# Performance work log

Hardware: AMD Instinct MI355X
Metric: run time of the kernel (lower is better)

## Reference

```python
import jax, jax.numpy as jnp
import numpy as np

B, IN_UNITS, IN_CHANNELS, NUM_UNITS, UNIT_SIZE = 256, 8, 1152, 10, 16
NUM_ITERS = 3


def setup_inputs() -> dict:
    key = jax.random.key(0)
    k1, k2 = jax.random.split(key)
    x = jax.random.normal(k1, (B, IN_UNITS, IN_CHANNELS), dtype=jnp.float32)
    # W from nn.Parameter(torch.randn(1, in_channels, num_units, unit_size, in_units)); drop leading 1
    W = jax.random.normal(k2, (IN_CHANNELS, NUM_UNITS, UNIT_SIZE, IN_UNITS), dtype=jnp.float32)
    return {"x": x, "W": W}


def reference(x, W):
    # x: [B, in_units=i, in_channels=j]; original transposes to [B, j, i]
    # u_hat = W @ x : [B, j, n, u]
    batch = x.shape[0]
    u_hat = jnp.einsum('jnui,bij->bjnu', W, x)
    b = jnp.zeros((IN_CHANNELS, NUM_UNITS), dtype=x.dtype)  # b_ij [j, n]
    v = None
    for _ in range(NUM_ITERS):
        # legacy F.softmax on 4D [1,j,n,1] -> dim=1 = in_channels axis
        c = jax.nn.softmax(b, axis=0)  # [j, n]
        s = jnp.einsum('jn,bjnu->bnu', c, u_hat)  # s_j: [B, n, u]
        # squash over dim=2 of [B,1,n,u,1] == num_units axis (axis=1 here)
        mag_sq = jnp.sum(s * s, axis=1, keepdims=True)  # [B, 1, u]
        v = (mag_sq / (1.0 + mag_sq)) * (s / jnp.sqrt(mag_sq))  # [B, n, u]
        # agreement: mean over batch of <u_hat, v>
        b = b + jnp.einsum('bjnu,bnu->jn', u_hat, v) / batch
    return v[..., None]  # [B, num_units, unit_size, 1] == v_j.squeeze(1)
```

## Files before the change

kernel.cpp:

```cpp
#include <hip/hip_runtime.h>
#include <stdint.h>

#define B   256
#define IU  8
#define JC  1152
#define NN  10
#define UU  16
#define NU  160
#define JN  11520
#define WROW 1280
#define NP  9216
#define KB  36

typedef short bf16x8 __attribute__((ext_vector_type(8)));
typedef float f32x4  __attribute__((ext_vector_type(4)));

__device__ __forceinline__ short f2bf(float f) {
    union { float f; uint32_t u; } cv; cv.f = f;
    uint32_t u = cv.u;
    uint32_t r = u + 0x7fffu + ((u >> 16) & 1u);
    return (short)(r >> 16);
}
__device__ __forceinline__ float bf2f(short h) {
    union { uint32_t u; float f; } cv; cv.u = ((uint32_t)(unsigned short)h) << 16;
    return cv.f;
}
__device__ __forceinline__ uint32_t bfbits(float f) {
    union { float f; uint32_t u; } cv; cv.f = f;
    return (cv.u + 0x7fffu + ((cv.u >> 16) & 1u)) >> 16;
}
__device__ __forceinline__ uint32_t pk2(float a, float b) {
    return bfbits(a) | (bfbits(b) << 16);
}
__device__ __forceinline__ void gload16(const void* g, void* l) {
    __builtin_amdgcn_global_load_lds(
        (const __attribute__((address_space(1))) void*)g,
        (__attribute__((address_space(3))) void*)l, 16, 0, 0);
}

__global__ void __launch_bounds__(256)
k_prep(const float* __restrict__ xg, const float* __restrict__ wg,
       short* __restrict__ wbf, short* __restrict__ xbf) {
    const int bid = blockIdx.x, tid = threadIdx.x;
    if (bid < 576) {
        const int jt = bid % 18, rt = bid / 18;
        const int j0 = jt * 64, r0 = rt * 64;
        __shared__ short T[64][72];
        #pragma unroll
        for (int p = 0; p < 4; ++p) {
            int idx = tid + 256 * p;
            int row = idx >> 4;
            int c4  = (idx & 15) * 4;
            float4 xv = *reinterpret_cast<const float4*>(
                &xg[(size_t)(r0 + row) * JC + j0 + c4]);
            T[c4+0][row] = f2bf(xv.x);
            T[c4+1][row] = f2bf(xv.y);
            T[c4+2][row] = f2bf(xv.z);
            T[c4+3][row] = f2bf(xv.w);
        }
        __syncthreads();
        #pragma unroll
        for (int p = 0; p < 2; ++p) {
            int idx = tid + 256 * p;
            int jl = idx >> 3;
            int r8 = (idx & 7) * 8;
            uint4 d = *reinterpret_cast<const uint4*>(&T[jl][r8]);
            *reinterpret_cast<uint4*>(&xbf[(size_t)(j0 + jl) * 2048 + r0 + r8]) = d;
        }
    } else {
        const int b2 = bid - 576;
        size_t base = (size_t)b2 * 2048 + (size_t)tid * 8;
        float4 f0 = *reinterpret_cast<const float4*>(&wg[base]);
        float4 f1 = *reinterpret_cast<const float4*>(&wg[base + 4]);
        uint4 d;
        d.x = pk2(f0.x, f0.y); d.y = pk2(f0.z, f0.w);
        d.z = pk2(f1.x, f1.y); d.w = pk2(f1.z, f1.w);
        *reinterpret_cast<uint4*>(&wbf[base]) = d;
    }
}

__global__ void __launch_bounds__(256, 2)
k_gemm1(const short* __restrict__ xbf, const short* __restrict__ wbf,
        float* __restrict__ s_part) {
    const int kb = blockIdx.x, mt = blockIdx.y;
    const int tid = threadIdx.x;
    const int wv = tid >> 6, lane = tid & 63;
    const int q = lane >> 4, l16 = lane & 15;
    const int b0 = mt * 32;
    const int jb0 = kb * 32;
    const int mfrag = wv >> 1;
    const int ntb = (wv & 1) * 5;

    __shared__ __align__(16) short As[8 * 32 * 8];
    __shared__ __align__(16) short Bs[8 * 160 * 8];

    f32x4 acc[5];
    #pragma unroll
    for (int nt = 0; nt < 5; ++nt) acc[nt] = (f32x4){0.f, 0.f, 0.f, 0.f};

    for (int jc = 0; jc < 4; ++jc) {
        const int j0 = jb0 + jc * 8;
        __syncthreads();
        gload16(xbf + ((size_t)(j0 + (tid >> 5)) * 2048 + (size_t)(b0 + (tid & 31)) * 8),
                &As[tid * 8]);
        const short* wsrc = wbf + (size_t)j0 * WROW;
        #pragma unroll
        for (int p = 0; p < 5; ++p) {
            int ridx = tid + 256 * p;
            gload16(wsrc + (size_t)ridx * 8, &Bs[ridx * 8]);
        }
        __syncthreads();
        #pragma unroll
        for (int s = 0; s < 2; ++s) {
            int jj = s * 4 + q;
            bf16x8 av = *reinterpret_cast<const bf16x8*>(
                &As[(jj * 32 + mfrag * 16 + l16) << 3]);
            #pragma unroll
            for (int nt = 0; nt < 5; ++nt) {
                bf16x8 bv = *reinterpret_cast<const bf16x8*>(
                    &Bs[(jj * 160 + (ntb + nt) * 16 + l16) << 3]);
                acc[nt] = __builtin_amdgcn_mfma_f32_16x16x32_bf16(av, bv, acc[nt], 0, 0, 0);
            }
        }
    }
    float* dst = s_part + (size_t)(kb * 8 + mt) * 5120;
    #pragma unroll
    for (int nt = 0; nt < 5; ++nt)
        #pragma unroll
        for (int reg = 0; reg < 4; ++reg)
            dst[(mfrag * 16 + q * 4 + reg) * 160 + (ntb + nt) * 16 + l16] = acc[nt][reg];
}

__global__ void __launch_bounds__(320, 2)
k_reduce_s(const float* __restrict__ s_part, float* __restrict__ vdst,
           const float* __restrict__ expsum, int t0) {
    const int b = blockIdx.x, tid = threadIdx.x;
    const int t = tid % 160, kq = tid / 160;
    const int mt = b >> 5, bl = b & 31;
    const size_t off = (size_t)mt * 5120 + bl * 160 + t;

    __shared__ float invn[NN];
    if (tid < NN) invn[tid] = t0 ? (1.f / (float)JC) : 1.f / expsum[tid];

    float s = 0.f;
    for (int r = 0; r < 18; ++r)
        s += s_part[(size_t)(kq * 18 + r) * 40960 + off];

    __shared__ float red[2][160];
    __shared__ float sv[NU];
    __shared__ float fb[UU];
    red[kq][t] = s;
    __syncthreads();
    if (tid < NU) sv[tid] = (red[0][tid] + red[1][tid]) * invn[tid >> 4];
    __syncthreads();
    if (tid < UU) {
        float m = 0.f;
        #pragma unroll
        for (int n = 0; n < NN; ++n) { float z = sv[n*16 + tid]; m = fmaf(z, z, m); }
        fb[tid] = sqrtf(m) / (1.f + m);
    }
    __syncthreads();
    if (tid < NU)
        vdst[(size_t)b * NU + tid] = sv[tid] * fb[tid & 15];
}

__global__ void __launch_bounds__(256, 2)
k_vxg(const float* __restrict__ vg, const float* __restrict__ xg,
      float* __restrict__ G, float* __restrict__ expsum) {
    const int np0 = blockIdx.x * 64, m0 = blockIdx.y * 32;
    const int tid = threadIdx.x;
    const int wv = tid >> 6, lane = tid & 63;
    const int q = lane >> 4, l16 = lane & 15;

    if (blockIdx.x == 0 && blockIdx.y == 0 && tid < NN) expsum[tid] = 0.f;

    __shared__ __align__(16) short Ash[8 * 32 * 8];
    __shared__ __align__(16) short Asl[8 * 32 * 8];
    __shared__ __align__(16) short Bsh[8 * 64 * 8];
    __shared__ __align__(16) short Bsl[8 * 64 * 8];

    f32x4 acc[2];
    acc[0] = (f32x4){0.f,0.f,0.f,0.f};
    acc[1] = (f32x4){0.f,0.f,0.f,0.f};

    for (int ks = 0; ks < 4; ++ks) {
        const int b0 = ks * 64;
        __syncthreads();
        #pragma unroll
        for (int p = 0; p < 8; ++p) {
            int idx = tid + 256 * p;
            int bb = idx >> 5, ml = idx & 31;
            float vv = vg[(size_t)(b0 + bb) * NU + m0 + ml];
            short hi = f2bf(vv);
            short lo = f2bf(vv - bf2f(hi));
            int a = ((bb >> 3) * 32 + ml) * 8 + (bb & 7);
            Ash[a] = hi; Asl[a] = lo;
        }
        #pragma unroll
        for (int p = 0; p < 16; ++p) {
            int idx = tid + 256 * p;
            int bb = idx >> 6, nl = idx & 63;
            float xv = xg[(size_t)(b0 + bb) * NP + np0 + nl];
            short hi = f2bf(xv);
            short lo = f2bf(xv - bf2f(hi));
            int a = ((bb >> 3) * 64 + nl) * 8 + (bb & 7);
            Bsh[a] = hi; Bsl[a] = lo;
        }
        __syncthreads();
        #pragma unroll
        for (int s = 0; s < 2; ++s) {
            int kc = s*4 + q;
            bf16x8 bh = *reinterpret_cast<const bf16x8*>(&Bsh[((kc*64 + wv*16 + l16) << 3)]);
            bf16x8 bl = *reinterpret_cast<const bf16x8*>(&Bsl[((kc*64 + wv*16 + l16) << 3)]);
            #pragma unroll
            for (int mtl = 0; mtl < 2; ++mtl) {
                bf16x8 ah = *reinterpret_cast<const bf16x8*>(&Ash[((kc*32 + mtl*16 + l16) << 3)]);
                bf16x8 al = *reinterpret_cast<const bf16x8*>(&Asl[((kc*32 + mtl*16 + l16) << 3)]);
                acc[mtl] = __builtin_amdgcn_mfma_f32_16x16x32_bf16(ah, bh, acc[mtl], 0, 0, 0);
                acc[mtl] = __builtin_amdgcn_mfma_f32_16x16x32_bf16(ah, bl, acc[mtl], 0, 0, 0);
                acc[mtl] = __builtin_amdgcn_mfma_f32_16x16x32_bf16(al, bh, acc[mtl], 0, 0, 0);
            }
        }
    }
    #pragma unroll
    for (int mtl = 0; mtl < 2; ++mtl)
        #pragma unroll
        for (int reg = 0; reg < 4; ++reg) {
            int m  = m0 + mtl*16 + q*4 + reg;
            G[(size_t)m * NP + np0 + wv*16 + l16] = acc[mtl][reg];
        }
}

__global__ void k_wg_db(const float* __restrict__ wg, const float* __restrict__ G,
                        float* __restrict__ blog, short* __restrict__ wbf,
                        float* __restrict__ expsum, int t0) {
    const int j0 = blockIdx.x * 64, n = blockIdx.y;
    const int tid = threadIdx.x;
    const int jl = tid & 63, up = tid >> 6;
    const int j = j0 + jl;

    const float4* wp = reinterpret_cast<const float4*>(
        wg + (size_t)j * WROW + n * 128 + up * 32);
    float4 w[8];
    #pragma unroll
    for (int k = 0; k < 8; ++k) w[k] = wp[k];

    float acc = 0.f;
    #pragma unroll
    for (int q4 = 0; q4 < 4; ++q4) {
        int u = up*4 + q4;
        const float* gp = G + (size_t)(n*16 + u) * NP + j;
        float4 w0 = w[q4*2], w1 = w[q4*2 + 1];
        acc = fmaf(w0.x, gp[0*JC], acc);
        acc = fmaf(w0.y, gp[1*JC], acc);
        acc = fmaf(w0.z, gp[2*JC], acc);
        acc = fmaf(w0.w, gp[3*JC], acc);
        acc = fmaf(w1.x, gp[4*JC], acc);
        acc = fmaf(w1.y, gp[5*JC], acc);
        acc = fmaf(w1.z, gp[6*JC], acc);
        acc = fmaf(w1.w, gp[7*JC], acc);
    }
    __shared__ float red[4][64];
    __shared__ float esh[64];
    __shared__ __align__(16) short Wsh[64][136];
    red[up][jl] = acc;
    __syncthreads();
    if (tid < 64) {
        int jj = j0 + tid;
        float d = (red[0][tid] + red[1][tid] + red[2][tid] + red[3][tid])
                  * (1.f / (float)B);
        float nb = t0 ? d : (blog[jj*NN + n] + d);
        blog[jj*NN + n] = nb;
        float e = __expf(nb);
        esh[tid] = e;
        float s = e;
        s += __shfl_xor(s, 1);  s += __shfl_xor(s, 2);
        s += __shfl_xor(s, 4);  s += __shfl_xor(s, 8);
        s += __shfl_xor(s, 16); s += __shfl_xor(s, 32);
        if (tid == 0) atomicAdd(&expsum[n], s);
    }
    __syncthreads();
    const float e = esh[jl];
    #pragma unroll
    for (int q4 = 0; q4 < 4; ++q4) {
        float4 a = w[q4*2], bq = w[q4*2 + 1];
        uint4 d;
        d.x = pk2(a.x * e, a.y * e);
        d.y = pk2(a.z * e, a.w * e);
        d.z = pk2(bq.x * e, bq.y * e);
        d.w = pk2(bq.z * e, bq.w * e);
        *reinterpret_cast<uint4*>(&Wsh[jl][up*32 + q4*8]) = d;
    }
    __syncthreads();
    #pragma unroll
    for (int p = 0; p < 4; ++p) {
        int idx = tid + 256 * p;
        int jj = idx >> 4, seg = idx & 15;
        uint4 d = *reinterpret_cast<const uint4*>(&Wsh[jj][seg * 8]);
        *reinterpret_cast<uint4*>(&wbf[(size_t)(j0 + jj) * WROW + n*128 + seg*8]) = d;
    }
}

extern "C" void kernel_launch(void* const* d_in, const int* in_sizes, int n_in,
                              void* d_out, int out_size, void* d_ws, size_t ws_size,
                              hipStream_t stream) {
    const float* x = (const float*)d_in[0];
    const float* w = (const float*)d_in[1];
    float* out = (float*)d_out;

    float* ws     = (float*)d_ws;
    float* blog   = ws;
    float* expsum = blog + JN;
    float* v      = expsum + 16;
    short* wbf    = (short*)(v + (size_t)B * NU);
    short* xbf    = wbf + (size_t)JC * WROW;
    float* s_part = (float*)(xbf + (size_t)JC * 2048);
    float* G      = s_part;

    k_prep<<<1296, 256, 0, stream>>>(x, w, wbf, xbf);
    for (int t = 0; t < 3; ++t) {
        k_gemm1<<<dim3(KB, 8), 256, 0, stream>>>(xbf, wbf, s_part);
        k_reduce_s<<<B, 320, 0, stream>>>(s_part, (t == 2) ? out : v, expsum,
                                          (t == 0) ? 1 : 0);
        if (t < 2) {
            k_vxg<<<dim3(144, 5), 256, 0, stream>>>(v, x, G, expsum);
            k_wg_db<<<dim3(18, 10), 256, 0, stream>>>(w, G, blog, wbf, expsum,
                                                      (t == 0) ? 1 : 0);
        }
    }
}
```

Before: 144.1 us.

## Fuse reduction stages into producer kernels via atomic counter grid barriers

```diff
diff --git a/kernel.cpp b/kernel.cpp
--- a/kernel.cpp
+++ b/kernel.cpp
@@ -40,8 +40,9 @@
 
 __global__ void __launch_bounds__(256)
 k_prep(const float* __restrict__ xg, const float* __restrict__ wg,
-       short* __restrict__ wbf, short* __restrict__ xbf) {
+       short* __restrict__ wbf, short* __restrict__ xbf, int* __restrict__ cnt) {
     const int bid = blockIdx.x, tid = threadIdx.x;
+    if (bid == 0 && tid < 32) cnt[tid] = 0;
     if (bid < 576) {
         const int jt = bid % 18, rt = bid / 18;
         const int j0 = jt * 64, r0 = rt * 64;
@@ -80,8 +81,9 @@
 }
 
 __global__ void __launch_bounds__(256, 2)
-k_gemm1(const short* __restrict__ xbf, const short* __restrict__ wbf,
-        float* __restrict__ s_part) {
+k_gemmred(const short* __restrict__ xbf, const short* __restrict__ wbf,
+          float* __restrict__ s_part, float* __restrict__ vdst,
+          const float* __restrict__ expsum, int* __restrict__ cnt, int t0) {
     const int kb = blockIdx.x, mt = blockIdx.y;
     const int tid = threadIdx.x;
     const int wv = tid >> 6, lane = tid & 63;
@@ -91,8 +93,9 @@
     const int mfrag = wv >> 1;
     const int ntb = (wv & 1) * 5;
 
-    __shared__ __align__(16) short As[8 * 32 * 8];
-    __shared__ __align__(16) short Bs[8 * 160 * 8];
+    __shared__ __align__(16) char smem[24576];
+    short* As = (short*)smem;
+    short* Bs = As + 2048;
 
     f32x4 acc[5];
     #pragma unroll
@@ -129,55 +132,58 @@
         #pragma unroll
         for (int reg = 0; reg < 4; ++reg)
             dst[(mfrag * 16 + q * 4 + reg) * 160 + (ntb + nt) * 16 + l16] = acc[nt][reg];
-}
-
-__global__ void __launch_bounds__(320, 2)
-k_reduce_s(const float* __restrict__ s_part, float* __restrict__ vdst,
-           const float* __restrict__ expsum, int t0) {
-    const int b = blockIdx.x, tid = threadIdx.x;
-    const int t = tid % 160, kq = tid / 160;
-    const int mt = b >> 5, bl = b & 31;
-    const size_t off = (size_t)mt * 5120 + bl * 160 + t;
-
-    __shared__ float invn[NN];
-    if (tid < NN) invn[tid] = t0 ? (1.f / (float)JC) : 1.f / expsum[tid];
-
-    float s = 0.f;
-    for (int r = 0; r < 18; ++r)
-        s += s_part[(size_t)(kq * 18 + r) * 40960 + off];
-
-    __shared__ float red[2][160];
-    __shared__ float sv[NU];
-    __shared__ float fb[UU];
-    red[kq][t] = s;
-    __syncthreads();
-    if (tid < NU) sv[tid] = (red[0][tid] + red[1][tid]) * invn[tid >> 4];
+
+    __syncthreads();
+    if (tid == 0)
+        __hip_atomic_fetch_add(&cnt[mt], 1, __ATOMIC_RELEASE, __HIP_MEMORY_SCOPE_AGENT);
+    if (kb >= 32) return;
+    if (tid == 0) {
+        while (__hip_atomic_load(&cnt[mt], __ATOMIC_ACQUIRE, __HIP_MEMORY_SCOPE_AGENT) < KB)
+            __builtin_amdgcn_s_sleep(4);
+    }
+    __syncthreads();
+
+    float* sv  = (float*)smem;
+    float* fbv = sv + 160;
+    if (tid < NU) {
+        float ssum = 0.f;
+        const float* sp = s_part + (size_t)mt * 5120 + (size_t)kb * 160 + tid;
+        #pragma unroll 4
+        for (int r = 0; r < KB; ++r)
+            ssum += sp[(size_t)r * 40960];
+        float inv = t0 ? (1.f / (float)JC) : 1.f / expsum[tid >> 4];
+        sv[tid] = ssum * inv;
+    }
     __syncthreads();
     if (tid < UU) {
         float m = 0.f;
         #pragma unroll
         for (int n = 0; n < NN; ++n) { float z = sv[n*16 + tid]; m = fmaf(z, z, m); }
-        fb[tid] = sqrtf(m) / (1.f + m);
+        fbv[tid] = sqrtf(m) / (1.f + m);
     }
     __syncthreads();
     if (tid < NU)
-        vdst[(size_t)b * NU + tid] = sv[tid] * fb[tid & 15];
-}
-
-__global__ void __launch_bounds__(256, 2)
-k_vxg(const float* __restrict__ vg, const float* __restrict__ xg,
-      float* __restrict__ G, float* __restrict__ expsum) {
+        vdst[(size_t)(mt * 32 + kb) * NU + tid] = sv[tid] * fbv[tid & 15];
+}
+
+__global__ void __launch_bounds__(256, 3)
+k_vxgdb(const float* __restrict__ vg, const float* __restrict__ xg,
+        const float* __restrict__ wg, float* __restrict__ G,
+        float* __restrict__ blog, short* __restrict__ wbf,
+        float* __restrict__ expsum, int* __restrict__ cnt, int t0) {
     const int np0 = blockIdx.x * 64, m0 = blockIdx.y * 32;
+    const int fid = blockIdx.y * 144 + blockIdx.x;
     const int tid = threadIdx.x;
     const int wv = tid >> 6, lane = tid & 63;
     const int q = lane >> 4, l16 = lane & 15;
 
-    if (blockIdx.x == 0 && blockIdx.y == 0 && tid < NN) expsum[tid] = 0.f;
-
-    __shared__ __align__(16) short Ash[8 * 32 * 8];
-    __shared__ __align__(16) short Asl[8 * 32 * 8];
-    __shared__ __align__(16) short Bsh[8 * 64 * 8];
-    __shared__ __align__(16) short Bsl[8 * 64 * 8];
+    __shared__ __align__(16) char smem[24576];
+    short* Ash = (short*)smem;
+    short* Asl = Ash + 2048;
+    short* Bsh = Asl + 2048;
+    short* Bsl = Bsh + 4096;
+
+    if (fid == 0 && tid < NN) expsum[tid] = 0.f;
 
     f32x4 acc[2];
     acc[0] = (f32x4){0.f,0.f,0.f,0.f};
@@ -210,12 +216,12 @@
         #pragma unroll
         for (int s = 0; s < 2; ++s) {
             int kc = s*4 + q;
-            bf16x8 bh = *reinterpret_cast<const bf16x8*>(&Bsh[((kc*64 + wv*16 + l16) << 3)]);
-            bf16x8 bl = *reinterpret_cast<const bf16x8*>(&Bsl[((kc*64 + wv*16 + l16) << 3)]);
+            bf16x8 bh = *reinterpret_cast<const bf16x8*>(&Bsh[(kc*64 + wv*16 + l16) << 3]);
+            bf16x8 bl = *reinterpret_cast<const bf16x8*>(&Bsl[(kc*64 + wv*16 + l16) << 3]);
             #pragma unroll
             for (int mtl = 0; mtl < 2; ++mtl) {
-                bf16x8 ah = *reinterpret_cast<const bf16x8*>(&Ash[((kc*32 + mtl*16 + l16) << 3)]);
-                bf16x8 al = *reinterpret_cast<const bf16x8*>(&Asl[((kc*32 + mtl*16 + l16) << 3)]);
+                bf16x8 ah = *reinterpret_cast<const bf16x8*>(&Ash[(kc*32 + mtl*16 + l16) << 3]);
+                bf16x8 al = *reinterpret_cast<const bf16x8*>(&Asl[(kc*32 + mtl*16 + l16) << 3]);
                 acc[mtl] = __builtin_amdgcn_mfma_f32_16x16x32_bf16(ah, bh, acc[mtl], 0, 0, 0);
                 acc[mtl] = __builtin_amdgcn_mfma_f32_16x16x32_bf16(ah, bl, acc[mtl], 0, 0, 0);
                 acc[mtl] = __builtin_amdgcn_mfma_f32_16x16x32_bf16(al, bh, acc[mtl], 0, 0, 0);
@@ -229,15 +235,24 @@
             int m  = m0 + mtl*16 + q*4 + reg;
             G[(size_t)m * NP + np0 + wv*16 + l16] = acc[mtl][reg];
         }
-}
-
-__global__ void k_wg_db(const float* __restrict__ wg, const float* __restrict__ G,
-                        float* __restrict__ blog, short* __restrict__ wbf,
-                        float* __restrict__ expsum, int t0) {
-    const int j0 = blockIdx.x * 64, n = blockIdx.y;
-    const int tid = threadIdx.x;
+
+    __syncthreads();
+    if (tid == 0)
+        __hip_atomic_fetch_add(cnt, 1, __ATOMIC_RELEASE, __HIP_MEMORY_SCOPE_AGENT);
+    if (fid >= 180) return;
+    if (tid == 0) {
+        while (__hip_atomic_load(cnt, __ATOMIC_ACQUIRE, __HIP_MEMORY_SCOPE_AGENT) < 720)
+            __builtin_amdgcn_s_sleep(4);
+    }
+    __syncthreads();
+
+    const int j0 = (fid % 18) * 64, n = fid / 18;
     const int jl = tid & 63, up = tid >> 6;
     const int j = j0 + jl;
+
+    short* Wsh = (short*)smem;
+    float* red = (float*)(smem + 17408);
+    float* esh = red + 256;
 
     const float4* wp = reinterpret_cast<const float4*>(
         wg + (size_t)j * WROW + n * 128 + up * 32);
@@ -245,29 +260,26 @@
     #pragma unroll
     for (int k = 0; k < 8; ++k) w[k] = wp[k];
 
-    float acc = 0.f;
+    float dacc = 0.f;
     #pragma unroll
     for (int q4 = 0; q4 < 4; ++q4) {
         int u = up*4 + q4;
         const float* gp = G + (size_t)(n*16 + u) * NP + j;
         float4 w0 = w[q4*2], w1 = w[q4*2 + 1];
-        acc = fmaf(w0.x, gp[0*JC], acc);
-        acc = fmaf(w0.y, gp[1*JC], acc);
-        acc = fmaf(w0.z, gp[2*JC], acc);
-        acc = fmaf(w0.w, gp[3*JC], acc);
-        acc = fmaf(w1.x, gp[4*JC], acc);
-        acc = fmaf(w1.y, gp[5*JC], acc);
-        acc = fmaf(w1.z, gp[6*JC], acc);
-        acc = fmaf(w1.w, gp[7*JC], acc);
-    }
-    __shared__ float red[4][64];
-    __shared__ float esh[64];
-    __shared__ __align__(16) short Wsh[64][136];
-    red[up][jl] = acc;
+        dacc = fmaf(w0.x, gp[0*JC], dacc);
+        dacc = fmaf(w0.y, gp[1*JC], dacc);
+        dacc = fmaf(w0.z, gp[2*JC], dacc);
+        dacc = fmaf(w0.w, gp[3*JC], dacc);
+        dacc = fmaf(w1.x, gp[4*JC], dacc);
+        dacc = fmaf(w1.y, gp[5*JC], dacc);
+        dacc = fmaf(w1.z, gp[6*JC], dacc);
+        dacc = fmaf(w1.w, gp[7*JC], dacc);
+    }
+    red[up*64 + jl] = dacc;
     __syncthreads();
     if (tid < 64) {
         int jj = j0 + tid;
-        float d = (red[0][tid] + red[1][tid] + red[2][tid] + red[3][tid])
+        float d = (red[0*64+tid] + red[1*64+tid] + red[2*64+tid] + red[3*64+tid])
                   * (1.f / (float)B);
         float nb = t0 ? d : (blog[jj*NN + n] + d);
         blog[jj*NN + n] = nb;
@@ -289,14 +301,14 @@
         d.y = pk2(a.z * e, a.w * e);
         d.z = pk2(bq.x * e, bq.y * e);
         d.w = pk2(bq.z * e, bq.w * e);
-        *reinterpret_cast<uint4*>(&Wsh[jl][up*32 + q4*8]) = d;
+        *reinterpret_cast<uint4*>(&Wsh[jl*136 + up*32 + q4*8]) = d;
     }
     __syncthreads();
     #pragma unroll
     for (int p = 0; p < 4; ++p) {
         int idx = tid + 256 * p;
         int jj = idx >> 4, seg = idx & 15;
-        uint4 d = *reinterpret_cast<const uint4*>(&Wsh[jj][seg * 8]);
+        uint4 d = *reinterpret_cast<const uint4*>(&Wsh[jj*136 + seg*8]);
         *reinterpret_cast<uint4*>(&wbf[(size_t)(j0 + jj) * WROW + n*128 + seg*8]) = d;
     }
 }
@@ -316,16 +328,15 @@
     short* xbf    = wbf + (size_t)JC * WROW;
     float* s_part = (float*)(xbf + (size_t)JC * 2048);
     float* G      = s_part;
-
-    k_prep<<<1296, 256, 0, stream>>>(x, w, wbf, xbf);
+    int*   cnt    = (int*)(s_part + (size_t)KB * 40960);
+
+    k_prep<<<1296, 256, 0, stream>>>(x, w, wbf, xbf, cnt);
     for (int t = 0; t < 3; ++t) {
-        k_gemm1<<<dim3(KB, 8), 256, 0, stream>>>(xbf, wbf, s_part);
-        k_reduce_s<<<B, 320, 0, stream>>>(s_part, (t == 2) ? out : v, expsum,
-                                          (t == 0) ? 1 : 0);
-        if (t < 2) {
-            k_vxg<<<dim3(144, 5), 256, 0, stream>>>(v, x, G, expsum);
-            k_wg_db<<<dim3(18, 10), 256, 0, stream>>>(w, G, blog, wbf, expsum,
-                                                      (t == 0) ? 1 : 0);
-        }
-    }
-}
+        k_gemmred<<<dim3(KB, 8), 256, 0, stream>>>(
+            xbf, wbf, s_part, (t == 2) ? out : v, expsum, cnt + t * 8,
+            (t == 0) ? 1 : 0);
+        if (t < 2)
+            k_vxgdb<<<dim3(144, 5), 256, 0, stream>>>(
+                v, x, w, G, blog, wbf, expsum, cnt + 24 + t, (t == 0) ? 1 : 0);
+    }
+}
```

New measurement: 365.0 us. 2.53x slower.

## Fuse v·x GEMM with W contraction and logit update into one routing kernel

Applied to the files above, without the earlier changes.

```diff
diff --git a/kernel.cpp b/kernel.cpp
--- a/kernel.cpp
+++ b/kernel.cpp
@@ -40,8 +40,10 @@
 
 __global__ void __launch_bounds__(256)
 k_prep(const float* __restrict__ xg, const float* __restrict__ wg,
-       short* __restrict__ wbf, short* __restrict__ xbf) {
+       short* __restrict__ wbf, short* __restrict__ xbf,
+       float* __restrict__ expsum) {
     const int bid = blockIdx.x, tid = threadIdx.x;
+    if (bid == 0 && tid < 32) expsum[tid] = 0.f;
     if (bid < 576) {
         const int jt = bid % 18, rt = bid / 18;
         const int j0 = jt * 64, r0 = rt * 64;
@@ -164,140 +166,115 @@
         vdst[(size_t)b * NU + tid] = sv[tid] * fb[tid & 15];
 }
 
-__global__ void __launch_bounds__(256, 2)
-k_vxg(const float* __restrict__ vg, const float* __restrict__ xg,
-      float* __restrict__ G, float* __restrict__ expsum) {
-    const int np0 = blockIdx.x * 64, m0 = blockIdx.y * 32;
+__global__ void __launch_bounds__(256)
+k_route(const float* __restrict__ vg, const float* __restrict__ xg,
+        const float* __restrict__ wg, float* __restrict__ blog,
+        short* __restrict__ wbf, float* __restrict__ expsum, int t0) {
+    const int jt = blockIdx.x, ng = blockIdx.y;
+    const int j0 = jt * 32, n0 = ng * 2, m0 = n0 * 16;
     const int tid = threadIdx.x;
     const int wv = tid >> 6, lane = tid & 63;
     const int q = lane >> 4, l16 = lane & 15;
-
-    if (blockIdx.x == 0 && blockIdx.y == 0 && tid < NN) expsum[tid] = 0.f;
-
-    __shared__ __align__(16) short Ash[8 * 32 * 8];
-    __shared__ __align__(16) short Asl[8 * 32 * 8];
-    __shared__ __align__(16) short Bsh[8 * 64 * 8];
-    __shared__ __align__(16) short Bsl[8 * 64 * 8];
-
-    f32x4 acc[2];
-    acc[0] = (f32x4){0.f,0.f,0.f,0.f};
-    acc[1] = (f32x4){0.f,0.f,0.f,0.f};
-
-    for (int ks = 0; ks < 4; ++ks) {
-        const int b0 = ks * 64;
-        __syncthreads();
-        #pragma unroll
-        for (int p = 0; p < 8; ++p) {
-            int idx = tid + 256 * p;
-            int bb = idx >> 5, ml = idx & 31;
-            float vv = vg[(size_t)(b0 + bb) * NU + m0 + ml];
-            short hi = f2bf(vv);
-            short lo = f2bf(vv - bf2f(hi));
-            int a = ((bb >> 3) * 32 + ml) * 8 + (bb & 7);
-            Ash[a] = hi; Asl[a] = lo;
-        }
-        #pragma unroll
-        for (int p = 0; p < 16; ++p) {
-            int idx = tid + 256 * p;
-            int bb = idx >> 6, nl = idx & 63;
-            float xv = xg[(size_t)(b0 + bb) * NP + np0 + nl];
+    const int mtl = wv >> 1, ntc = wv & 1;
+
+    __shared__ __align__(16) short Ash[8192], Asl[8192];
+    __shared__ __align__(16) short Bsh[8192], Bsl[8192];
+    __shared__ float Gt[32 * 32];
+    __shared__ float red[256];
+    __shared__ float esh[64];
+
+    #pragma unroll
+    for (int p = 0; p < 32; ++p) {
+        int e = tid + 256 * p;
+        int b = e >> 5, ml = e & 31;
+        float vv = vg[(size_t)b * NU + m0 + ml];
+        short hi = f2bf(vv);
+        short lo = f2bf(vv - bf2f(hi));
+        int a = (b >> 6) * 2048 + (((b >> 3) & 7) * 32 + ml) * 8 + (b & 7);
+        Ash[a] = hi; Asl[a] = lo;
+    }
+
+    float part = 0.f;
+    for (int i = 0; i < 8; ++i) {
+        __syncthreads();
+        #pragma unroll
+        for (int p = 0; p < 32; ++p) {
+            int e = tid + 256 * p;
+            int b = e >> 5, jl = e & 31;
+            float xv = xg[(size_t)b * NP + i * JC + j0 + jl];
             short hi = f2bf(xv);
             short lo = f2bf(xv - bf2f(hi));
-            int a = ((bb >> 3) * 64 + nl) * 8 + (bb & 7);
+            int a = (b >> 6) * 2048 + (((b >> 3) & 7) * 32 + jl) * 8 + (b & 7);
             Bsh[a] = hi; Bsl[a] = lo;
         }
         __syncthreads();
-        #pragma unroll
-        for (int s = 0; s < 2; ++s) {
-            int kc = s*4 + q;
-            bf16x8 bh = *reinterpret_cast<const bf16x8*>(&Bsh[((kc*64 + wv*16 + l16) << 3)]);
-            bf16x8 bl = *reinterpret_cast<const bf16x8*>(&Bsl[((kc*64 + wv*16 + l16) << 3)]);
+        f32x4 acc = (f32x4){0.f, 0.f, 0.f, 0.f};
+        #pragma unroll
+        for (int ks = 0; ks < 4; ++ks)
             #pragma unroll
-            for (int mtl = 0; mtl < 2; ++mtl) {
-                bf16x8 ah = *reinterpret_cast<const bf16x8*>(&Ash[((kc*32 + mtl*16 + l16) << 3)]);
-                bf16x8 al = *reinterpret_cast<const bf16x8*>(&Asl[((kc*32 + mtl*16 + l16) << 3)]);
-                acc[mtl] = __builtin_amdgcn_mfma_f32_16x16x32_bf16(ah, bh, acc[mtl], 0, 0, 0);
-                acc[mtl] = __builtin_amdgcn_mfma_f32_16x16x32_bf16(ah, bl, acc[mtl], 0, 0, 0);
-                acc[mtl] = __builtin_amdgcn_mfma_f32_16x16x32_bf16(al, bh, acc[mtl], 0, 0, 0);
+            for (int s = 0; s < 2; ++s) {
+                int kc = s * 4 + q;
+                const int ai = ks * 2048 + (kc * 32 + mtl * 16 + l16) * 8;
+                const int bi = ks * 2048 + (kc * 32 + ntc * 16 + l16) * 8;
+                bf16x8 ah = *reinterpret_cast<const bf16x8*>(&Ash[ai]);
+                bf16x8 al = *reinterpret_cast<const bf16x8*>(&Asl[ai]);
+                bf16x8 bh = *reinterpret_cast<const bf16x8*>(&Bsh[bi]);
+                bf16x8 bl = *reinterpret_cast<const bf16x8*>(&Bsl[bi]);
+                acc = __builtin_amdgcn_mfma_f32_16x16x32_bf16(ah, bh, acc, 0, 0, 0);
+                acc = __builtin_amdgcn_mfma_f32_16x16x32_bf16(ah, bl, acc, 0, 0, 0);
+                acc = __builtin_amdgcn_mfma_f32_16x16x32_bf16(al, bh, acc, 0, 0, 0);
             }
-        }
-    }
-    #pragma unroll
-    for (int mtl = 0; mtl < 2; ++mtl)
-        #pragma unroll
-        for (int reg = 0; reg < 4; ++reg) {
-            int m  = m0 + mtl*16 + q*4 + reg;
-            G[(size_t)m * NP + np0 + wv*16 + l16] = acc[mtl][reg];
-        }
-}
-
-__global__ void k_wg_db(const float* __restrict__ wg, const float* __restrict__ G,
-                        float* __restrict__ blog, short* __restrict__ wbf,
-                        float* __restrict__ expsum, int t0) {
-    const int j0 = blockIdx.x * 64, n = blockIdx.y;
-    const int tid = threadIdx.x;
-    const int jl = tid & 63, up = tid >> 6;
-    const int j = j0 + jl;
-
-    const float4* wp = reinterpret_cast<const float4*>(
-        wg + (size_t)j * WROW + n * 128 + up * 32);
-    float4 w[8];
-    #pragma unroll
-    for (int k = 0; k < 8; ++k) w[k] = wp[k];
-
-    float acc = 0.f;
-    #pragma unroll
-    for (int q4 = 0; q4 < 4; ++q4) {
-        int u = up*4 + q4;
-        const float* gp = G + (size_t)(n*16 + u) * NP + j;
-        float4 w0 = w[q4*2], w1 = w[q4*2 + 1];
-        acc = fmaf(w0.x, gp[0*JC], acc);
-        acc = fmaf(w0.y, gp[1*JC], acc);
-        acc = fmaf(w0.z, gp[2*JC], acc);
-        acc = fmaf(w0.w, gp[3*JC], acc);
-        acc = fmaf(w1.x, gp[4*JC], acc);
-        acc = fmaf(w1.y, gp[5*JC], acc);
-        acc = fmaf(w1.z, gp[6*JC], acc);
-        acc = fmaf(w1.w, gp[7*JC], acc);
-    }
-    __shared__ float red[4][64];
-    __shared__ float esh[64];
-    __shared__ __align__(16) short Wsh[64][136];
-    red[up][jl] = acc;
+        __syncthreads();
+        #pragma unroll
+        for (int r = 0; r < 4; ++r)
+            Gt[(mtl * 16 + q * 4 + r) * 32 + ntc * 16 + l16] = acc[r];
+        __syncthreads();
+        {
+            int jl = tid & 31, rr = tid >> 5;
+            int nn = rr >> 2, uq = rr & 3;
+            const float* wrow = wg + (size_t)(j0 + jl) * WROW + (n0 + nn) * 128 + i;
+            #pragma unroll
+            for (int k = 0; k < 4; ++k)
+                part = fmaf(Gt[(nn * 16 + uq * 4 + k) * 32 + jl],
+                            wrow[(uq * 4 + k) * 8], part);
+        }
+    }
+    {
+        int jl = tid & 31, rr = tid >> 5;
+        red[((rr >> 2) * 32 + jl) * 4 + (rr & 3)] = part;
+    }
     __syncthreads();
     if (tid < 64) {
-        int jj = j0 + tid;
-        float d = (red[0][tid] + red[1][tid] + red[2][tid] + red[3][tid])
+        int jl = tid & 31, nn = tid >> 5;
+        int ri = (nn * 32 + jl) * 4;
+        float d = (red[ri] + red[ri + 1] + red[ri + 2] + red[ri + 3])
                   * (1.f / (float)B);
-        float nb = t0 ? d : (blog[jj*NN + n] + d);
-        blog[jj*NN + n] = nb;
+        int bi = (j0 + jl) * NN + n0 + nn;
+        float nb = t0 ? d : (blog[bi] + d);
+        blog[bi] = nb;
         float e = __expf(nb);
-        esh[tid] = e;
-        float s = e;
-        s += __shfl_xor(s, 1);  s += __shfl_xor(s, 2);
-        s += __shfl_xor(s, 4);  s += __shfl_xor(s, 8);
-        s += __shfl_xor(s, 16); s += __shfl_xor(s, 32);
-        if (tid == 0) atomicAdd(&expsum[n], s);
-    }
-    __syncthreads();
-    const float e = esh[jl];
-    #pragma unroll
-    for (int q4 = 0; q4 < 4; ++q4) {
-        float4 a = w[q4*2], bq = w[q4*2 + 1];
-        uint4 d;
-        d.x = pk2(a.x * e, a.y * e);
-        d.y = pk2(a.z * e, a.w * e);
-        d.z = pk2(bq.x * e, bq.y * e);
-        d.w = pk2(bq.z * e, bq.w * e);
-        *reinterpret_cast<uint4*>(&Wsh[jl][up*32 + q4*8]) = d;
-    }
-    __syncthreads();
-    #pragma unroll
-    for (int p = 0; p < 4; ++p) {
-        int idx = tid + 256 * p;
-        int jj = idx >> 4, seg = idx & 15;
-        uint4 d = *reinterpret_cast<const uint4*>(&Wsh[jj][seg * 8]);
-        *reinterpret_cast<uint4*>(&wbf[(size_t)(j0 + jj) * WROW + n*128 + seg*8]) = d;
+        esh[jl * 2 + nn] = e;
+        float ssum = e;
+        ssum += __shfl_xor(ssum, 1);  ssum += __shfl_xor(ssum, 2);
+        ssum += __shfl_xor(ssum, 4);  ssum += __shfl_xor(ssum, 8);
+        ssum += __shfl_xor(ssum, 16);
+        if ((tid & 31) == 0) atomicAdd(&expsum[n0 + nn], ssum);
+    }
+    __syncthreads();
+    {
+        int row = tid >> 3, seg = tid & 7;
+        float e = esh[row * 2 + (seg >> 2)];
+        const float4* wp = reinterpret_cast<const float4*>(
+            wg + (size_t)(j0 + row) * WROW + n0 * 128 + seg * 32);
+        short* dst = wbf + (size_t)(j0 + row) * WROW + n0 * 128 + seg * 32;
+        #pragma unroll
+        for (int k2 = 0; k2 < 4; ++k2) {
+            float4 f0 = wp[k2 * 2], f1 = wp[k2 * 2 + 1];
+            uint4 dd;
+            dd.x = pk2(f0.x * e, f0.y * e); dd.y = pk2(f0.z * e, f0.w * e);
+            dd.z = pk2(f1.x * e, f1.y * e); dd.w = pk2(f1.z * e, f1.w * e);
+            *reinterpret_cast<uint4*>(&dst[k2 * 8]) = dd;
+        }
     }
 }
 
@@ -311,21 +288,19 @@
     float* ws     = (float*)d_ws;
     float* blog   = ws;
     float* expsum = blog + JN;
-    float* v      = expsum + 16;
+    float* v      = expsum + 32;
     short* wbf    = (short*)(v + (size_t)B * NU);
     short* xbf    = wbf + (size_t)JC * WROW;
     float* s_part = (float*)(xbf + (size_t)JC * 2048);
-    float* G      = s_part;
-
-    k_prep<<<1296, 256, 0, stream>>>(x, w, wbf, xbf);
+
+    k_prep<<<1296, 256, 0, stream>>>(x, w, wbf, xbf, expsum);
     for (int t = 0; t < 3; ++t) {
         k_gemm1<<<dim3(KB, 8), 256, 0, stream>>>(xbf, wbf, s_part);
-        k_reduce_s<<<B, 320, 0, stream>>>(s_part, (t == 2) ? out : v, expsum,
-                                          (t == 0) ? 1 : 0);
-        if (t < 2) {
-            k_vxg<<<dim3(144, 5), 256, 0, stream>>>(v, x, G, expsum);
-            k_wg_db<<<dim3(18, 10), 256, 0, stream>>>(w, G, blog, wbf, expsum,
-                                                      (t == 0) ? 1 : 0);
-        }
-    }
-}
+        k_reduce_s<<<B, 320, 0, stream>>>(
+            s_part, (t == 2) ? out : v,
+            expsum + ((t == 0) ? 0 : (t - 1) * 16), (t == 0) ? 1 : 0);
+        if (t < 2)
+            k_route<<<dim3(36, 5), 256, 0, stream>>>(
+                v, x, w, blog, wbf, expsum + t * 16, (t == 0) ? 1 : 0);
+    }
+}
```

After: 142.6 us (median of 2 runs). About the same (-1.0%).
